# Performance work log

Hardware: AMD Instinct MI355X
Metric: run time of the kernel (lower is better)

Reference implementation:

```python
import jax, jax.numpy as jnp
import numpy as np

N = 4096          # num_nodes
E = 131072        # num_edges (avg degree 32)
H = 32            # hidden_channels
C_IN, C_OUT = 3, 3
DEPTH = 4
KS = [2000, 1000, 500, 250]  # ceil(ratio * n) per level, ratios = [2000/N, .5, .5, .5]


def gcn(x, A, W, b):
    """GCNConv with improved=True (self-loop fill 2, preserved if already present),
    symmetric normalization, aggregation out[dst] += norm * h[src]."""
    d = jnp.diagonal(A)
    A_hat = A + jnp.diag(jnp.where(d > 0, 0.0, 2.0))
    deg = A_hat.sum(0)                       # in-degree (col sums), as gcn_norm
    dis = jnp.where(deg > 0, jax.lax.rsqrt(deg), 0.0)
    msg = (x @ W) * dis[:, None]
    return (A_hat.T @ msg) * dis[:, None] + b


def augment(A):
    """GraphUNet.augment_adj: add self loops (w=1), square adjacency, drop self loops."""
    n = A.shape[0]
    eye = jnp.eye(n, dtype=A.dtype)
    A_sl = A + eye
    return (A_sl @ A_sl) * (1.0 - eye)


def pool(x, A, p, k):
    """TopKPooling: score = tanh((x.p)/||p||), keep top-k, gate x by score."""
    score = jnp.tanh((x @ p) / jnp.linalg.norm(p))
    vals, perm = jax.lax.top_k(score, k)
    return x[perm] * vals[:, None], A[perm][:, perm], perm


def setup_inputs() -> dict:
    key = jax.random.key(0)
    ks = jax.random.split(key, 12)
    x = jax.random.normal(ks[0], (N, C_IN), jnp.float32)
    edge_index = jax.random.randint(ks[1], (2, E), 0, N, dtype=jnp.int64)
    s = 0.1
    return {
        "x": x,
        "edge_index": edge_index,
        "W0": jax.random.normal(ks[2], (C_IN, H)) * s,
        "b0": jnp.zeros((H,), jnp.float32),
        "Wd": jax.random.normal(ks[3], (DEPTH, H, H)) * s,
        "bd": jnp.zeros((DEPTH, H), jnp.float32),
        "P": jax.random.normal(ks[4], (DEPTH, H)) * s,
        "Wu": jax.random.normal(ks[5], (DEPTH - 1, H, H)) * s,
        "bu": jnp.zeros((DEPTH - 1, H), jnp.float32),
        "Wlast": jax.random.normal(ks[6], (H, C_OUT)) * s,
        "blast": jnp.zeros((C_OUT,), jnp.float32),
    }


def reference(x, edge_index, W0, b0, Wd, bd, P, Wu, bu, Wlast, blast):
    # dense adjacency; duplicate edges accumulate like coalesced sparse weights
    A = jnp.zeros((N, N), jnp.float32).at[edge_index[0], edge_index[1]].add(1.0)
    x = jax.nn.relu(gcn(x, A, W0, b0))
    xs, As, perms = [x], [A], []
    for i in range(DEPTH):
        A = augment(A)
        x, A, perm = pool(x, A, P[i], KS[i])
        x = jax.nn.relu(gcn(x, A, Wd[i], bd[i]))
        if i < DEPTH - 1:
            xs.append(x)
            As.append(A)
        perms.append(perm)
    for i in range(DEPTH):
        j = DEPTH - 1 - i
        res = xs[j]
        up = jnp.zeros_like(res).at[perms[j]].set(x)  # unpool
        x = res + up                                   # sum_res=True
        if i < DEPTH - 1:
            x = jax.nn.relu(gcn(x, As[j], Wu[i], bu[i]))
        else:
            x = gcn(x, As[j], Wlast, blast)
    return jax.nn.log_softmax(x, axis=1)
```

## Files before the change

### kernel.cpp

```cpp
#include <hip/hip_runtime.h>
#include <math.h>

#define H 32
#define N0 4096
#define EMAX 131072
#define APSTR (4096 * 32)

typedef __attribute__((ext_vector_type(4))) float floatx4;
typedef __attribute__((ext_vector_type(8))) short short8;

__device__ __forceinline__ unsigned short f2bf_bits(float v) {
    union { float f; unsigned u; } c;
    c.f = v;
    unsigned lsb = (c.u >> 16) & 1u;
    c.u += 0x7fffu + lsb;
    return (unsigned short)(c.u >> 16);
}

__global__ void fill_sentinel_kernel(float* out, int n) {
    int t = blockIdx.x * 256 + threadIdx.x;
    if (t < n) out[t] = 9.0f;
}

__global__ void build_stats_kernel(const int* __restrict__ ei, int E, int* __restrict__ rowcnt,
                                   int* __restrict__ rowcntD, int* __restrict__ diagcnt) {
    int t = blockIdx.x * 256 + threadIdx.x;
    if (t >= E) return;
    int s = ei[t], d = ei[E + t];
    if ((unsigned)s >= N0 || (unsigned)d >= N0) return;
    atomicAdd(&rowcnt[s], 1);
    atomicAdd(&rowcntD[d], 1);
    if (s == d) atomicAdd(&diagcnt[s], 1);
}

__global__ __launch_bounds__(1024) void scan2_kernel(const int* __restrict__ cntA, int* __restrict__ rowpA,
                                                     int* __restrict__ curA, const int* __restrict__ cntB,
                                                     int* __restrict__ rowpB, int* __restrict__ curB) {
    __shared__ int part[1024];
    int tid = threadIdx.x;
    for (int pass = 0; pass < 2; pass++) {
        const int* cnt = pass ? cntB : cntA;
        int* rowp = pass ? rowpB : rowpA;
        int* cur = pass ? curB : curA;
        int base = tid * 4;
        int local[4];
        int s = 0;
#pragma unroll
        for (int i = 0; i < 4; i++) { local[i] = s; s += cnt[base + i]; }
        part[tid] = s;
        __syncthreads();
        for (int off = 1; off < 1024; off <<= 1) {
            int v = (tid >= off) ? part[tid - off] : 0;
            __syncthreads();
            part[tid] += v;
            __syncthreads();
        }
        int pre = (tid == 0) ? 0 : part[tid - 1];
#pragma unroll
        for (int i = 0; i < 4; i++) { rowp[base + i] = pre + local[i]; cur[base + i] = pre + local[i]; }
        if (tid == 1023) rowp[N0] = pre + s;
        __syncthreads();
    }
}

__global__ void fill_csr_kernel(const int* __restrict__ ei, int E, int* __restrict__ cursor,
                                int* __restrict__ cols, int* __restrict__ cursorD,
                                int* __restrict__ srcs) {
    int t = blockIdx.x * 256 + threadIdx.x;
    if (t >= E) return;
    int s = ei[t], d = ei[E + t];
    if ((unsigned)s >= N0 || (unsigned)d >= N0) return;
    int pos = atomicAdd(&cursor[s], 1);
    cols[pos] = d;
    int posD = atomicAdd(&cursorD[d], 1);
    srcs[posD] = s;
}

__global__ void invperm_set_kernel(const int* __restrict__ perm, int* __restrict__ invperm, int k) {
    int t = blockIdx.x * 256 + threadIdx.x;
    if (t < k) invperm[perm[t]] = t;
}

__global__ __launch_bounds__(256) void aug0_kernel(const int* __restrict__ rowp, const int* __restrict__ cols,
                                                   const int* __restrict__ perm, const int* __restrict__ invperm,
                                                   int kOut, int ldC, float* __restrict__ C) {
    __shared__ float row[2048];
    int a = blockIdx.x;
    int tid = threadIdx.x;
    for (int j = tid; j < ldC; j += 256) row[j] = 0.f;
    __syncthreads();
    if (a < kOut) {
        int pa = perm[a];
        int s0 = rowp[pa], s1 = rowp[pa + 1];
        for (int e = s0 + tid; e < s1; e += 256) {
            int k = cols[e];
            int ip = invperm[k];
            if (ip >= 0) atomicAdd(&row[ip], 2.0f);
            int t1 = rowp[k + 1];
            for (int e2 = rowp[k]; e2 < t1; ++e2) {
                int ip2 = invperm[cols[e2]];
                if (ip2 >= 0) atomicAdd(&row[ip2], 1.0f);
            }
        }
    }
    __syncthreads();
    for (int j = tid; j < ldC; j += 256) C[(long)a * ldC + j] = (j == a) ? 0.f : row[j];
}

__global__ void gather_rows_kernel(const float* __restrict__ M, int ldM, const int* __restrict__ perm,
                                   int kOut, float* __restrict__ Gr) {
    int k = blockIdx.x * 256 + threadIdx.x;
    int a = blockIdx.y;
    if (k >= ldM) return;
    float v = 0.f;
    if (a < kOut) {
        int pa = perm[a];
        v = M[(long)pa * ldM + k] + (k == pa ? 1.f : 0.f);
    }
    Gr[(long)a * ldM + k] = v;
}

__global__ void gather_rows_bf16_kernel(const float* __restrict__ M, int ldM, const int* __restrict__ perm,
                                        int kOut, unsigned short* __restrict__ Gr) {
    int k = blockIdx.x * 256 + threadIdx.x;
    int a = blockIdx.y;
    if (k >= ldM) return;
    float v = 0.f;
    if (a < kOut) {
        int pa = perm[a];
        v = M[(long)pa * ldM + k] + (k == pa ? 1.f : 0.f);
    }
    Gr[(long)a * ldM + k] = f2bf_bits(v);
}

__global__ void gather_cols_kernel(const float* __restrict__ M, int ldM, const int* __restrict__ perm,
                                   int kOut, float* __restrict__ Gc, int ldC) {
    int b = blockIdx.x * 256 + threadIdx.x;
    int k = blockIdx.y;
    if (b >= ldC) return;
    float v = 0.f;
    if (b < kOut) {
        int pb = perm[b];
        v = M[(long)k * ldM + pb] + (k == pb ? 1.f : 0.f);
    }
    Gc[(long)k * ldC + b] = v;
}

__global__ void gather_colsT_bf16_kernel(const float* __restrict__ M, int ldM,
                                         const int* __restrict__ perm, int kOut,
                                         unsigned short* __restrict__ GcT) {
    __shared__ float t[32][33];
    __shared__ int pb[32];
    int b0 = blockIdx.x * 32, k0 = blockIdx.y * 32;
    int tx = threadIdx.x, ty = threadIdx.y;
    if (ty == 0) pb[tx] = (b0 + tx < kOut) ? perm[b0 + tx] : -1;
    __syncthreads();
    for (int y = ty; y < 32; y += 8) {
        int k = k0 + y;
        int pbx = pb[tx];
        float v = 0.f;
        if (pbx >= 0) v = M[(long)k * ldM + pbx] + (k == pbx ? 1.f : 0.f);
        t[y][tx] = v;
    }
    __syncthreads();
    for (int y = ty; y < 32; y += 8)
        GcT[(long)(b0 + y) * ldM + k0 + tx] = f2bf_bits(t[tx][y]);
}

__global__ __launch_bounds__(256) void mfma_aug_kernel(const unsigned short* __restrict__ Aop,
                                                       const unsigned short* __restrict__ Bop,
                                                       float* __restrict__ C, int K, int ldC, int kchunk) {
    __shared__ __align__(16) unsigned short lA[64 * 32];
    __shared__ __align__(16) unsigned short lB[64 * 32];
    const int tid = threadIdx.x;
    const int lane = tid & 63;
    const int w = tid >> 6;
    const int a0 = blockIdx.y * 64, b0 = blockIdx.x * 64;
    const int kbase = blockIdx.z * kchunk;
    const int r0 = tid >> 2;
    const int c8 = (tid & 3) * 8;
    const unsigned short* gA = Aop + (long)(a0 + r0) * K + kbase + c8;
    const unsigned short* gB = Bop + (long)(b0 + r0) * K + kbase + c8;
    const int wm = (w & 1) * 32;
    const int wn = (w >> 1) * 32;
    const int lm = lane & 15;
    const int quad = lane >> 4;
    floatx4 acc[2][2];
#pragma unroll
    for (int i = 0; i < 2; i++)
#pragma unroll
        for (int j = 0; j < 2; j++) {
            floatx4 z = {0.f, 0.f, 0.f, 0.f};
            acc[i][j] = z;
        }
    for (int k0 = 0; k0 < kchunk; k0 += 32) {
        short8 va = *(const short8*)(gA + k0);
        short8 vb = *(const short8*)(gB + k0);
        __syncthreads();
        *(short8*)&lA[r0 * 32 + c8] = va;
        *(short8*)&lB[r0 * 32 + c8] = vb;
        __syncthreads();
        short8 af[2], bf[2];
#pragma unroll
        for (int mi = 0; mi < 2; mi++) af[mi] = *(const short8*)&lA[(wm + mi * 16 + lm) * 32 + quad * 8];
#pragma unroll
        for (int ni = 0; ni < 2; ni++) bf[ni] = *(const short8*)&lB[(wn + ni * 16 + lm) * 32 + quad * 8];
#pragma unroll
        for (int mi = 0; mi < 2; mi++)
#pragma unroll
            for (int ni = 0; ni < 2; ni++)
                acc[mi][ni] = __builtin_amdgcn_mfma_f32_16x16x32_bf16(af[mi], bf[ni], acc[mi][ni], 0, 0, 0);
    }
#pragma unroll
    for (int mi = 0; mi < 2; mi++)
#pragma unroll
        for (int ni = 0; ni < 2; ni++) {
            int col = b0 + wn + ni * 16 + lm;
#pragma unroll
            for (int r = 0; r < 4; r++) {
                int row = a0 + wm + mi * 16 + quad * 4 + r;
                if (row != col) atomicAdd(&C[(long)row * ldC + col], acc[mi][ni][r]);
            }
        }
}

__global__ __launch_bounds__(256) void gemm64_kernel(const float* __restrict__ Gr,
                                                     const float* __restrict__ Gc,
                                                     float* __restrict__ Cpart, int K, int ldC, int kchunk) {
    __shared__ float As[32][68];
    __shared__ float Bs[32][68];
    const int tid = threadIdx.x;
    const int a0 = blockIdx.y * 64, b0 = blockIdx.x * 64;
    const int kbase = blockIdx.z * kchunk;
    float* Cz = Cpart + (long)blockIdx.z * ldC * ldC;
    const int tx = tid & 15, ty = tid >> 4;
    const int lr = tid >> 2;
    const int lk = (tid & 3) * 8;
    const int bb = tid & 63;
    const int kr = (tid >> 6) * 8;
    const float* gA = Gr + (long)(a0 + lr) * K + lk + kbase;
    const float* gB = Gc + (long)(kr + kbase) * ldC + b0 + bb;
    float acc[4][4];
#pragma unroll
    for (int i = 0; i < 4; i++)
#pragma unroll
        for (int j = 0; j < 4; j++) acc[i][j] = 0.f;
    for (int k0 = 0; k0 < kchunk; k0 += 32) {
        float a8[8], b8[8];
#pragma unroll
        for (int i = 0; i < 8; i++) a8[i] = gA[k0 + i];
#pragma unroll
        for (int i = 0; i < 8; i++) b8[i] = gB[(long)(k0 + i) * ldC];
        __syncthreads();
#pragma unroll
        for (int i = 0; i < 8; i++) As[lk + i][lr] = a8[i];
#pragma unroll
        for (int i = 0; i < 8; i++) Bs[kr + i][bb] = b8[i];
        __syncthreads();
#pragma unroll
        for (int k = 0; k < 32; k++) {
            floatx4 av = *(const floatx4*)&As[k][ty * 4];
            floatx4 bv = *(const floatx4*)&Bs[k][tx * 4];
#pragma unroll
            for (int i = 0; i < 4; i++)
#pragma unroll
                for (int j = 0; j < 4; j++) acc[i][j] += av[i] * bv[j];
        }
    }
#pragma unroll
    for (int i = 0; i < 4; i++)
#pragma unroll
        for (int j = 0; j < 4; j++) {
            int a = a0 + ty * 4 + i, b = b0 + tx * 4 + j;
            Cz[(long)a * ldC + b] = acc[i][j];
        }
}

__global__ void reduce_part_kernel(const float* __restrict__ Cpart, float* __restrict__ C,
                                   int ldC, int ksplit) {
    int t = blockIdx.x * 256 + threadIdx.x;
    long tot = (long)ldC * ldC;
    if (t >= tot) return;
    float s = 0.f;
    for (int z = 0; z < ksplit; z++) s += Cpart[(long)z * tot + t];
    int a = t / ldC, b = t % ldC;
    C[t] = (a == b) ? 0.f : s;
}

__global__ void colsum_part_kernel(const float* __restrict__ A, float* __restrict__ degp, int ld) {
    int i = blockIdx.x * 256 + threadIdx.x;
    int jb = blockIdx.y;
    int j0 = jb * 64;
    float s0 = 0.f, s1 = 0.f, s2 = 0.f, s3 = 0.f, s4 = 0.f, s5 = 0.f, s6 = 0.f, s7 = 0.f;
    const float* p = A + (long)j0 * ld + i;
#pragma unroll
    for (int jq = 0; jq < 64; jq += 8) {
        float v[8];
#pragma unroll
        for (int q = 0; q < 8; q++) v[q] = p[(long)(jq + q) * ld];
        s0 += v[0]; s1 += v[1]; s2 += v[2]; s3 += v[3];
        s4 += v[4]; s5 += v[5]; s6 += v[6]; s7 += v[7];
    }
    float s = ((s0 + s1) + (s2 + s3)) + ((s4 + s5) + (s6 + s7));
    degp[(long)jb * ld + i] = s;
}

__global__ void msgg_kernel(const float* __restrict__ x, const int* __restrict__ perm,
                            const float* __restrict__ vals, const float* __restrict__ Wb,
                            const float* __restrict__ A, int ld, const float* __restrict__ degp,
                            int nparts, float* __restrict__ dis, float* __restrict__ fixb,
                            float* __restrict__ msg, int n) {
    int idx = blockIdx.x * 256 + threadIdx.x;
    if (idx >= n * 32) return;
    int i = idx >> 5, c = idx & 31;
    float dsum = 0.f;
    for (int z = 0; z < nparts; z++) dsum += degp[(long)z * ld + i];
    float diag = A[(long)i * ld + i];
    float fx = diag > 0.f ? 0.f : 2.f;
    float dg = dsum + fx;
    float di = dg > 0.f ? 1.f / sqrtf(dg) : 0.f;
    if (c == 0) { dis[i] = di; fixb[i] = fx; }
    int src = perm ? perm[i] : i;
    float vs = vals ? vals[i] : 1.f;
    float s = 0.f;
#pragma unroll
    for (int q = 0; q < 32; q++) s += x[src * 32 + q] * Wb[q * 32 + c];
    msg[idx] = s * vs * di;
}

__global__ __launch_bounds__(256) void aggT_kernel(const float* __restrict__ A,
                                                   const float* __restrict__ msg,
                                                   float* __restrict__ aggp, int n, int ld, int jchunk) {
    __shared__ float As[64][64];
    __shared__ float Ms[64][32];
    const int tid = threadIdx.x;
    const int i0 = blockIdx.x * 64;
    const int il = tid & 63;
    const int cg = tid >> 6;
    const int i = i0 + il;
    const int mrow = tid >> 2;
    const int mc = (tid & 3) * 8;
    float acc[8];
#pragma unroll
    for (int q = 0; q < 8; q++) acc[q] = 0.f;
    const int j0 = blockIdx.y * jchunk;
    for (int jb = j0; jb < j0 + jchunk; jb += 64) {
        float a16[16], m8[8];
#pragma unroll
        for (int q = 0; q < 16; q++) a16[q] = A[(long)(jb + cg + 4 * q) * ld + i0 + il];
#pragma unroll
        for (int q = 0; q < 8; q++) m8[q] = msg[(long)(jb + mrow) * 32 + mc + q];
        __syncthreads();
#pragma unroll
        for (int q = 0; q < 16; q++) As[cg + 4 * q][il] = a16[q];
#pragma unroll
        for (int q = 0; q < 8; q++) Ms[mrow][mc + q] = m8[q];
        __syncthreads();
#pragma unroll
        for (int jl = 0; jl < 64; jl++) {
            float a = As[jl][il];
#pragma unroll
            for (int q = 0; q < 8; q++) acc[q] += a * Ms[jl][cg * 8 + q];
        }
        __syncthreads();
    }
    if (i < n) {
#pragma unroll
        for (int q = 0; q < 8; q++) aggp[(long)blockIdx.y * APSTR + (long)i * 32 + cg * 8 + q] = acc[q];
    }
}

__global__ void epi_sum_kernel(const float* __restrict__ aggp, int jsplit, const float* __restrict__ msg,
                               const float* __restrict__ dis, const float* __restrict__ fixb,
                               const float* __restrict__ bb, float* __restrict__ out, int n, int relu) {
    int idx = blockIdx.x * 256 + threadIdx.x;
    if (idx >= n * 32) return;
    int i = idx >> 5, c = idx & 31;
    float s = 0.f;
    for (int z = 0; z < jsplit; z++) s += aggp[(long)z * APSTR + idx];
    float v = (s + fixb[i] * msg[idx]) * dis[i] + bb[c];
    if (relu) v = fmaxf(v, 0.f);
    out[idx] = v;
}

__global__ void msg0_kernel(const float* __restrict__ x, const float* __restrict__ Wb,
                            const int* __restrict__ rowcntD, const int* __restrict__ diagcnt,
                            float* __restrict__ dis, float* __restrict__ fixb,
                            float* __restrict__ msg, int n) {
    int idx = blockIdx.x * 256 + threadIdx.x;
    if (idx >= n * 32) return;
    int i = idx >> 5, c = idx & 31;
    float fx = diagcnt[i] > 0 ? 0.f : 2.f;
    float dg = (float)rowcntD[i] + fx;
    float di = dg > 0.f ? 1.f / sqrtf(dg) : 0.f;
    if (c == 0) { dis[i] = di; fixb[i] = fx; }
    float s = x[i * 3] * Wb[c] + x[i * 3 + 1] * Wb[32 + c] + x[i * 3 + 2] * Wb[64 + c];
    msg[idx] = s * di;
}

template <int CIN, int COUT>
__global__ void msg_kernel(const float* __restrict__ x, const float* __restrict__ Wb,
                           const float* __restrict__ dis, float* __restrict__ msg, int n) {
    int idx = blockIdx.x * 256 + threadIdx.x;
    if (idx >= n * COUT) return;
    int i = idx / COUT, c = idx % COUT;
    float s = 0.f;
#pragma unroll
    for (int q = 0; q < CIN; q++) s += x[i * CIN + q] * Wb[q * COUT + c];
    msg[idx] = s * dis[i];
}

template <int COUT>
__global__ void cscagg_epi_kernel(const int* __restrict__ rowpD, const int* __restrict__ srcs,
                                  const float* __restrict__ msg, const float* __restrict__ dis,
                                  const float* __restrict__ fixb, const float* __restrict__ bb,
                                  float* __restrict__ out, int n, int relu) {
    int t = blockIdx.x * 256 + threadIdx.x;
    if (t >= n * COUT) return;
    int i = t / COUT, c = t % COUT;
    float acc = 0.f;
    int e0 = rowpD[i], e1 = rowpD[i + 1];
    for (int e = e0; e < e1; e++) acc += msg[(long)srcs[e] * COUT + c];
    float v = (acc + fixb[i] * msg[t]) * dis[i] + bb[c];
    if (relu) v = fmaxf(v, 0.f);
    out[t] = v;
}

__global__ void cscagg_lsm_kernel(const int* __restrict__ rowpD, const int* __restrict__ srcs,
                                  const float* __restrict__ msg, const float* __restrict__ dis,
                                  const float* __restrict__ fixb, const float* __restrict__ bb,
                                  float* __restrict__ out, int n) {
    int i = blockIdx.x * 256 + threadIdx.x;
    if (i >= n) return;
    float a0 = 0.f, a1 = 0.f, a2 = 0.f;
    int e0 = rowpD[i], e1 = rowpD[i + 1];
    for (int e = e0; e < e1; e++) {
        const float* m = &msg[(long)srcs[e] * 3];
        a0 += m[0]; a1 += m[1]; a2 += m[2];
    }
    float di = dis[i], fx = fixb[i];
    float v0 = (a0 + fx * msg[i * 3]) * di + bb[0];
    float v1 = (a1 + fx * msg[i * 3 + 1]) * di + bb[1];
    float v2 = (a2 + fx * msg[i * 3 + 2]) * di + bb[2];
    float m = fmaxf(v0, fmaxf(v1, v2));
    float s = expf(v0 - m) + expf(v1 - m) + expf(v2 - m);
    float l = m + logf(s);
    out[i * 3] = v0 - l;
    out[i * 3 + 1] = v1 - l;
    out[i * 3 + 2] = v2 - l;
}

__global__ void score_keys_kernel(const float* __restrict__ x, const float* __restrict__ p,
                                  int n, int npow, unsigned long long* __restrict__ keys) {
    __shared__ float psh[32];
    const int tid = threadIdx.x;
    if (tid < 32) psh[tid] = p[tid];
    __syncthreads();
    int i = blockIdx.x * 256 + tid;
    if (i >= npow) return;
    unsigned long long kk = 0ULL;
    if (i < n) {
        float nrm = 0.f, dot = 0.f;
#pragma unroll
        for (int c = 0; c < 32; c++) {
            nrm += psh[c] * psh[c];
            dot += x[i * 32 + c] * psh[c];
        }
        float sc = tanhf(dot / sqrtf(nrm));
        unsigned u = __float_as_uint(sc);
        u = (u & 0x80000000u) ? ~u : (u | 0x80000000u);
        kk = ((unsigned long long)u << 32) | (unsigned)(~i);
    }
    keys[i] = kk;
}

__global__ __launch_bounds__(256) void topk_rank_kernel(const unsigned long long* __restrict__ keys,
                                                        int npow, int k, int* __restrict__ perm,
                                                        float* __restrict__ vals) {
    __shared__ unsigned long long ks[4096];
    __shared__ int psum[256];
    const int tid = threadIdx.x;
    for (int t = tid; t < npow; t += 256) ks[t] = keys[t];
    __syncthreads();
    const int m = tid & 15;
    const int chunk = tid >> 4;
    const int myi = blockIdx.x * 16 + m;
    unsigned long long my = ks[myi];
    const int cl = npow >> 4;
    const unsigned long long* base = &ks[chunk * cl];
    int r = 0;
#pragma unroll 4
    for (int j = 0; j < cl; j++) r += (base[j] > my) ? 1 : 0;
    psum[chunk * 16 + m] = r;
    __syncthreads();
    if (tid < 16) {
        int mk_i = blockIdx.x * 16 + tid;
        unsigned long long mk = ks[mk_i];
        int rank = 0;
#pragma unroll
        for (int c = 0; c < 16; c++) rank += psum[c * 16 + tid];
        if (rank < k) {
            perm[rank] = (int)(~(unsigned)mk);
            unsigned u = (unsigned)(mk >> 32);
            u = (u & 0x80000000u) ? (u ^ 0x80000000u) : ~u;
            vals[rank] = __uint_as_float(u);
        }
    }
}

__global__ void copy_kernel(float* __restrict__ dst, const float* __restrict__ src, int n) {
    int t = blockIdx.x * 256 + threadIdx.x;
    if (t < n) dst[t] = src[t];
}

__global__ void scatter_add_kernel(float* __restrict__ dst, const float* __restrict__ src,
                                   const int* __restrict__ perm, int k) {
    int t = blockIdx.x * 256 + threadIdx.x;
    if (t >= k * H) return;
    int a = t >> 5, c = t & 31;
    dst[perm[a] * H + c] += src[t];
}

static void run_gcn_dense(hipStream_t st, const float* A, int n, int ld, const float* x,
                          const int* perm, const float* vals, const float* Wt, const float* bt,
                          int relu, float* out, float* degp, float* aggp, float* dis, float* fixb,
                          float* msgb) {
    dim3 gcs(ld / 256 > 0 ? ld / 256 : 1, ld / 64);
    colsum_part_kernel<<<gcs, 256, 0, st>>>(A, degp, ld);
    int gm = (n * H + 255) / 256;
    msgg_kernel<<<gm, 256, 0, st>>>(x, perm, vals, Wt, A, ld, degp, ld / 64, dis, fixb, msgb, n);
    int jsplit = ld / 256 > 0 ? ld / 256 : 1;
    int ajc = ld / jsplit;
    dim3 ga(ld / 64, jsplit);
    aggT_kernel<<<ga, 256, 0, st>>>(A, msgb, aggp, n, ld, ajc);
    epi_sum_kernel<<<gm, 256, 0, st>>>(aggp, jsplit, msgb, dis, fixb, bt, out, n, relu);
}

extern "C" void kernel_launch(void* const* d_in, const int* in_sizes, int n_in,
                              void* d_out, int out_size, void* d_ws, size_t ws_size,
                              hipStream_t stream) {
    const float* x0f = (const float*)d_in[0];
    const int* eidx = (const int*)d_in[1];
    const float* W0f = (const float*)d_in[2];
    const float* b0f = (const float*)d_in[3];
    const float* Wdf = (const float*)d_in[4];
    const float* bdf = (const float*)d_in[5];
    const float* Pf = (const float*)d_in[6];
    const float* Wuf = (const float*)d_in[7];
    const float* buf2 = (const float*)d_in[8];
    const float* Wlf = (const float*)d_in[9];
    const float* blf = (const float*)d_in[10];
    const int E = in_sizes[1] / 2;

    unsigned char* w = (unsigned char*)d_ws;
    size_t off = 0;
    auto alloc = [&](size_t bytes) -> void* {
        void* p = w + off;
        off += (bytes + 255) & ~(size_t)255;
        return p;
    };
    int* rowcnt = (int*)alloc(N0 * 4);
    int* rowcntD = (int*)alloc(N0 * 4);
    int* diagcnt = (int*)alloc(N0 * 4);
    int* rowp = (int*)alloc((N0 + 1) * 4);
    int* rowpD = (int*)alloc((N0 + 1) * 4);
    int* cursor = (int*)alloc(N0 * 4);
    int* cursorD = (int*)alloc(N0 * 4);
    int* cols = (int*)alloc((size_t)EMAX * 4);
    int* srcs = (int*)alloc((size_t)EMAX * 4);
    int* invperm = (int*)alloc(N0 * 4);
    float* dis0 = (float*)alloc(N0 * 4);
    float* fixb0 = (float*)alloc(N0 * 4);
    unsigned long long* keys = (unsigned long long*)alloc((size_t)N0 * 8);
    float* A1 = (float*)alloc((size_t)2048 * 2048 * 4);
    float* A2 = (float*)alloc((size_t)1024 * 1024 * 4);
    float* A3 = (float*)alloc((size_t)512 * 512 * 4);
    float* A4 = (float*)alloc((size_t)256 * 256 * 4);
    float* Gr = (float*)alloc((size_t)1024 * 2048 * 4);
    float* Gc = (float*)alloc((size_t)2048 * 1024 * 4);
    unsigned short* Grb = (unsigned short*)alloc((size_t)1024 * 2048 * 2);
    unsigned short* GcTb = (unsigned short*)alloc((size_t)1024 * 2048 * 2);
    float* Cpart = (float*)alloc((size_t)8 * 512 * 512 * 4);
    float* degp = (float*)alloc((size_t)32 * 2048 * 4);
    float* aggp = (float*)alloc((size_t)8 * APSTR * 4);
    float* xs0 = (float*)alloc((size_t)N0 * H * 4);
    float* xs1 = (float*)alloc((size_t)2000 * H * 4);
    float* xs2 = (float*)alloc((size_t)1000 * H * 4);
    float* xs3 = (float*)alloc((size_t)500 * H * 4);
    float* xtA = (float*)alloc((size_t)N0 * H * 4);
    float* xtB = (float*)alloc((size_t)N0 * H * 4);
    float* msgb = (float*)alloc((size_t)N0 * H * 4);
    float* dis = (float*)alloc(N0 * 4);
    float* fixb = (float*)alloc(N0 * 4);
    const int ksz[4] = {2000, 1000, 500, 250};
    int* perm[4];
    float* vals[4];
    for (int i = 0; i < 4; i++) perm[i] = (int*)alloc((size_t)ksz[i] * 4);
    for (int i = 0; i < 4; i++) vals[i] = (float*)alloc((size_t)ksz[i] * 4);

    if (off > ws_size) {
        fill_sentinel_kernel<<<(out_size + 255) / 256, 256, 0, stream>>>((float*)d_out, out_size);
        return;
    }

    const int nlvl[5] = {N0, 2000, 1000, 500, 250};
    const int ldl[5] = {N0, 2048, 1024, 512, 256};
    const int npw[4] = {4096, 2048, 1024, 512};
    float* Afp[5] = {nullptr, A1, A2, A3, A4};
    float* xsb[4] = {xs0, xs1, xs2, xs3};

    hipMemsetAsync(rowcnt, 0, (size_t)N0 * 3 * 4, stream);
    build_stats_kernel<<<(E + 255) / 256, 256, 0, stream>>>(eidx, E, rowcnt, rowcntD, diagcnt);
    scan2_kernel<<<1, 1024, 0, stream>>>(rowcnt, rowp, cursor, rowcntD, rowpD, cursorD);
    fill_csr_kernel<<<(E + 255) / 256, 256, 0, stream>>>(eidx, E, cursor, cols, cursorD, srcs);

    msg0_kernel<<<(N0 * H + 255) / 256, 256, 0, stream>>>(x0f, W0f, rowcntD, diagcnt, dis0, fixb0,
                                                          msgb, N0);
    cscagg_epi_kernel<H><<<(N0 * H + 255) / 256, 256, 0, stream>>>(rowpD, srcs, msgb, dis0, fixb0,
                                                                   b0f, xs0, N0, 1);
    float* xcur = xs0;

    for (int i = 0; i < 4; ++i) {
        int nd = nlvl[i], kk = ksz[i], ldn = ldl[i + 1];
        score_keys_kernel<<<(npw[i] + 255) / 256, 256, 0, stream>>>(xcur, Pf + i * H, nd, npw[i], keys);
        topk_rank_kernel<<<npw[i] / 16, 256, 0, stream>>>(keys, npw[i], kk, perm[i], vals[i]);
        if (i == 0) {
            hipMemsetAsync(invperm, 0xFF, (size_t)N0 * 4, stream);
            invperm_set_kernel<<<(kk + 255) / 256, 256, 0, stream>>>(perm[0], invperm, kk);
            aug0_kernel<<<ldn, 256, 0, stream>>>(rowp, cols, perm[0], invperm, kk, ldn, A1);
        } else if (i == 1) {
            int ldM = ldl[i];
            dim3 gr((ldM + 255) / 256, ldn);
            gather_rows_bf16_kernel<<<gr, 256, 0, stream>>>(Afp[i], ldM, perm[i], kk, Grb);
            dim3 gt(ldn / 32, ldM / 32);
            gather_colsT_bf16_kernel<<<gt, dim3(32, 8), 0, stream>>>(Afp[i], ldM, perm[i], kk, GcTb);
            hipMemsetAsync(Afp[i + 1], 0, (size_t)ldn * ldn * 4, stream);
            int ksplit = 4;
            int kchunk = ldM / ksplit;
            dim3 gg(ldn / 64, ldn / 64, ksplit);
            mfma_aug_kernel<<<gg, 256, 0, stream>>>(Grb, GcTb, Afp[i + 1], ldM, ldn, kchunk);
        } else {
            int ldM = ldl[i];
            dim3 gr((ldM + 255) / 256, ldn);
            gather_rows_kernel<<<gr, 256, 0, stream>>>(Afp[i], ldM, perm[i], kk, Gr);
            dim3 gc((ldn + 255) / 256, ldM);
            gather_cols_kernel<<<gc, 256, 0, stream>>>(Afp[i], ldM, perm[i], kk, Gc, ldn);
            int ksplit = 8;
            int kchunk = ldM / ksplit;
            dim3 gg(ldn / 64, ldn / 64, ksplit);
            gemm64_kernel<<<gg, 256, 0, stream>>>(Gr, Gc, Cpart, ldM, ldn, kchunk);
            long tot = (long)ldn * ldn;
            reduce_part_kernel<<<(tot + 255) / 256, 256, 0, stream>>>(Cpart, Afp[i + 1], ldn, ksplit);
        }
        float* outx = (i < 3) ? xsb[i + 1] : xtB;
        run_gcn_dense(stream, Afp[i + 1], kk, ldn, xcur, perm[i], vals[i], Wdf + i * (H * H),
                      bdf + i * H, 1, outx, degp, aggp, dis, fixb, msgb);
        xcur = outx;
    }

    for (int i = 0; i < 4; ++i) {
        int j = 3 - i;
        int nj = nlvl[j], kj = ksz[j];
        copy_kernel<<<(nj * H + 255) / 256, 256, 0, stream>>>(xtA, xsb[j], nj * H);
        scatter_add_kernel<<<(kj * H + 255) / 256, 256, 0, stream>>>(xtA, xcur, perm[j], kj);
        if (i < 3) {
            run_gcn_dense(stream, Afp[j], nj, ldl[j], xtA, nullptr, nullptr, Wuf + i * (H * H),
                          buf2 + i * H, 1, xtB, degp, aggp, dis, fixb, msgb);
        } else {
            msg_kernel<H, 3><<<(N0 * 3 + 255) / 256, 256, 0, stream>>>(xtA, Wlf, dis0, msgb, N0);
            cscagg_lsm_kernel<<<(N0 + 255) / 256, 256, 0, stream>>>(rowpD, srcs, msgb, dis0, fixb0,
                                                                    blf, (float*)d_out, N0);
        }
        xcur = xtB;
    }
}
```

Baseline: 477.5 us.

## Fuse TopK score computation into GCN epilogues and cache per-level degree normalization

The separate score_keys kernel is removed. Pooling scores and sort keys are now computed inside the GCN epilogue kernels using warp shuffles across the 32 channels, including padding entries up to the power-of-two size. Degree normalization (dis/fixb) is stored per level during the down pass and reused in the up pass, which skips the dense column-sum kernel and the diagonal read there. This removes several launches and full passes over dense adjacency matrices, at the cost of extra per-level buffers and a larger epilogue grid.

```diff
diff --git a/kernel.cpp b/kernel.cpp
--- a/kernel.cpp
+++ b/kernel.cpp
@@ -313,19 +313,26 @@
     int idx = blockIdx.x * 256 + threadIdx.x;
     if (idx >= n * 32) return;
     int i = idx >> 5, c = idx & 31;
-    float dsum = 0.f;
-    for (int z = 0; z < nparts; z++) dsum += degp[(long)z * ld + i];
-    float diag = A[(long)i * ld + i];
-    float fx = diag > 0.f ? 0.f : 2.f;
-    float dg = dsum + fx;
-    float di = dg > 0.f ? 1.f / sqrtf(dg) : 0.f;
-    if (c == 0) { dis[i] = di; fixb[i] = fx; }
+    float di, fx;
+    if (degp) {
+        float dsum = 0.f;
+        for (int z = 0; z < nparts; z++) dsum += degp[(long)z * ld + i];
+        float diag = A[(long)i * ld + i];
+        fx = diag > 0.f ? 0.f : 2.f;
+        float dg = dsum + fx;
+        di = dg > 0.f ? 1.f / sqrtf(dg) : 0.f;
+        if (c == 0) { dis[i] = di; fixb[i] = fx; }
+    } else {
+        di = dis[i];
+        fx = fixb[i];
+    }
     int src = perm ? perm[i] : i;
     float vs = vals ? vals[i] : 1.f;
     float s = 0.f;
 #pragma unroll
     for (int q = 0; q < 32; q++) s += x[src * 32 + q] * Wb[q * 32 + c];
     msg[idx] = s * vs * di;
+    (void)fx;
 }
 
 __global__ __launch_bounds__(256) void aggT_kernel(const float* __restrict__ A,
@@ -372,15 +379,46 @@
 
 __global__ void epi_sum_kernel(const float* __restrict__ aggp, int jsplit, const float* __restrict__ msg,
                                const float* __restrict__ dis, const float* __restrict__ fixb,
-                               const float* __restrict__ bb, float* __restrict__ out, int n, int relu) {
+                               const float* __restrict__ bb, float* __restrict__ out, int n, int relu,
+                               const float* __restrict__ p, int npow,
+                               unsigned long long* __restrict__ keys) {
+    __shared__ float psh[32];
+    if (p) {
+        if (threadIdx.x < 32) psh[threadIdx.x] = p[threadIdx.x];
+        __syncthreads();
+    }
     int idx = blockIdx.x * 256 + threadIdx.x;
-    if (idx >= n * 32) return;
+    int tot = (p ? npow : n) * 32;
+    if (idx >= tot) return;
     int i = idx >> 5, c = idx & 31;
-    float s = 0.f;
-    for (int z = 0; z < jsplit; z++) s += aggp[(long)z * APSTR + idx];
-    float v = (s + fixb[i] * msg[idx]) * dis[i] + bb[c];
-    if (relu) v = fmaxf(v, 0.f);
-    out[idx] = v;
+    float v = 0.f;
+    if (i < n) {
+        float s = 0.f;
+        for (int z = 0; z < jsplit; z++) s += aggp[(long)z * APSTR + idx];
+        v = (s + fixb[i] * msg[idx]) * dis[i] + bb[c];
+        if (relu) v = fmaxf(v, 0.f);
+        out[idx] = v;
+    }
+    if (p) {
+        float pc = psh[c];
+        float d = v * pc;
+        float nq = pc * pc;
+#pragma unroll
+        for (int st = 16; st >= 1; st >>= 1) {
+            d += __shfl_xor(d, st);
+            nq += __shfl_xor(nq, st);
+        }
+        if (c == 0) {
+            unsigned long long kk = 0ULL;
+            if (i < n) {
+                float sc = tanhf(d / sqrtf(nq));
+                unsigned u = __float_as_uint(sc);
+                u = (u & 0x80000000u) ? ~u : (u | 0x80000000u);
+                kk = ((unsigned long long)u << 32) | (unsigned)(~i);
+            }
+            keys[i] = kk;
+        }
+    }
 }
 
 __global__ void msg0_kernel(const float* __restrict__ x, const float* __restrict__ Wb,
@@ -410,20 +448,37 @@
     msg[idx] = s * dis[i];
 }
 
-template <int COUT>
-__global__ void cscagg_epi_kernel(const int* __restrict__ rowpD, const int* __restrict__ srcs,
-                                  const float* __restrict__ msg, const float* __restrict__ dis,
-                                  const float* __restrict__ fixb, const float* __restrict__ bb,
-                                  float* __restrict__ out, int n, int relu) {
-    int t = blockIdx.x * 256 + threadIdx.x;
-    if (t >= n * COUT) return;
-    int i = t / COUT, c = t % COUT;
+__global__ void cscagg_epi_keys_kernel(const int* __restrict__ rowpD, const int* __restrict__ srcs,
+                                       const float* __restrict__ msg, const float* __restrict__ dis,
+                                       const float* __restrict__ fixb, const float* __restrict__ bb,
+                                       float* __restrict__ out, int n, const float* __restrict__ p,
+                                       unsigned long long* __restrict__ keys) {
+    __shared__ float psh[32];
+    if (threadIdx.x < 32) psh[threadIdx.x] = p[threadIdx.x];
+    __syncthreads();
+    int idx = blockIdx.x * 256 + threadIdx.x;
+    if (idx >= n * 32) return;
+    int i = idx >> 5, c = idx & 31;
     float acc = 0.f;
     int e0 = rowpD[i], e1 = rowpD[i + 1];
-    for (int e = e0; e < e1; e++) acc += msg[(long)srcs[e] * COUT + c];
-    float v = (acc + fixb[i] * msg[t]) * dis[i] + bb[c];
-    if (relu) v = fmaxf(v, 0.f);
-    out[t] = v;
+    for (int e = e0; e < e1; e++) acc += msg[(long)srcs[e] * 32 + c];
+    float v = (acc + fixb[i] * msg[idx]) * dis[i] + bb[c];
+    v = fmaxf(v, 0.f);
+    out[idx] = v;
+    float pc = psh[c];
+    float d = v * pc;
+    float nq = pc * pc;
+#pragma unroll
+    for (int st = 16; st >= 1; st >>= 1) {
+        d += __shfl_xor(d, st);
+        nq += __shfl_xor(nq, st);
+    }
+    if (c == 0) {
+        float sc = tanhf(d / sqrtf(nq));
+        unsigned u = __float_as_uint(sc);
+        u = (u & 0x80000000u) ? ~u : (u | 0x80000000u);
+        keys[i] = ((unsigned long long)u << 32) | (unsigned)(~i);
+    }
 }
 
 __global__ void cscagg_lsm_kernel(const int* __restrict__ rowpD, const int* __restrict__ srcs,
@@ -448,30 +503,6 @@
     out[i * 3] = v0 - l;
     out[i * 3 + 1] = v1 - l;
     out[i * 3 + 2] = v2 - l;
-}
-
-__global__ void score_keys_kernel(const float* __restrict__ x, const float* __restrict__ p,
-                                  int n, int npow, unsigned long long* __restrict__ keys) {
-    __shared__ float psh[32];
-    const int tid = threadIdx.x;
-    if (tid < 32) psh[tid] = p[tid];
-    __syncthreads();
-    int i = blockIdx.x * 256 + tid;
-    if (i >= npow) return;
-    unsigned long long kk = 0ULL;
-    if (i < n) {
-        float nrm = 0.f, dot = 0.f;
-#pragma unroll
-        for (int c = 0; c < 32; c++) {
-            nrm += psh[c] * psh[c];
-            dot += x[i * 32 + c] * psh[c];
-        }
-        float sc = tanhf(dot / sqrtf(nrm));
-        unsigned u = __float_as_uint(sc);
-        u = (u & 0x80000000u) ? ~u : (u | 0x80000000u);
-        kk = ((unsigned long long)u << 32) | (unsigned)(~i);
-    }
-    keys[i] = kk;
 }
 
 __global__ __launch_bounds__(256) void topk_rank_kernel(const unsigned long long* __restrict__ keys,
@@ -524,16 +555,22 @@
 static void run_gcn_dense(hipStream_t st, const float* A, int n, int ld, const float* x,
                           const int* perm, const float* vals, const float* Wt, const float* bt,
                           int relu, float* out, float* degp, float* aggp, float* dis, float* fixb,
-                          float* msgb) {
-    dim3 gcs(ld / 256 > 0 ? ld / 256 : 1, ld / 64);
-    colsum_part_kernel<<<gcs, 256, 0, st>>>(A, degp, ld);
+                          float* msgb, int computeDeg, const float* pnext, int npow_next,
+                          unsigned long long* keys) {
+    if (computeDeg) {
+        dim3 gcs(ld / 256 > 0 ? ld / 256 : 1, ld / 64);
+        colsum_part_kernel<<<gcs, 256, 0, st>>>(A, degp, ld);
+    }
     int gm = (n * H + 255) / 256;
-    msgg_kernel<<<gm, 256, 0, st>>>(x, perm, vals, Wt, A, ld, degp, ld / 64, dis, fixb, msgb, n);
+    msgg_kernel<<<gm, 256, 0, st>>>(x, perm, vals, Wt, A, ld, computeDeg ? degp : nullptr, ld / 64,
+                                    dis, fixb, msgb, n);
     int jsplit = ld / 256 > 0 ? ld / 256 : 1;
     int ajc = ld / jsplit;
     dim3 ga(ld / 64, jsplit);
     aggT_kernel<<<ga, 256, 0, st>>>(A, msgb, aggp, n, ld, ajc);
-    epi_sum_kernel<<<gm, 256, 0, st>>>(aggp, jsplit, msgb, dis, fixb, bt, out, n, relu);
+    int gme = ((pnext ? npow_next : n) * H + 255) / 256;
+    epi_sum_kernel<<<gme, 256, 0, st>>>(aggp, jsplit, msgb, dis, fixb, bt, out, n, relu,
+                                        pnext, npow_next, keys);
 }
 
 extern "C" void kernel_launch(void* const* d_in, const int* in_sizes, int n_in,
@@ -590,8 +627,8 @@
     float* xtA = (float*)alloc((size_t)N0 * H * 4);
     float* xtB = (float*)alloc((size_t)N0 * H * 4);
     float* msgb = (float*)alloc((size_t)N0 * H * 4);
-    float* dis = (float*)alloc(N0 * 4);
-    float* fixb = (float*)alloc(N0 * 4);
+    float* disL = (float*)alloc((size_t)4 * N0 * 4);
+    float* fixbL = (float*)alloc((size_t)4 * N0 * 4);
     const int ksz[4] = {2000, 1000, 500, 250};
     int* perm[4];
     float* vals[4];
@@ -616,13 +653,12 @@
 
     msg0_kernel<<<(N0 * H + 255) / 256, 256, 0, stream>>>(x0f, W0f, rowcntD, diagcnt, dis0, fixb0,
                                                           msgb, N0);
-    cscagg_epi_kernel<H><<<(N0 * H + 255) / 256, 256, 0, stream>>>(rowpD, srcs, msgb, dis0, fixb0,
-                                                                   b0f, xs0, N0, 1);
+    cscagg_epi_keys_kernel<<<(N0 * H + 255) / 256, 256, 0, stream>>>(rowpD, srcs, msgb, dis0, fixb0,
+                                                                     b0f, xs0, N0, Pf, keys);
     float* xcur = xs0;
 
     for (int i = 0; i < 4; ++i) {
-        int nd = nlvl[i], kk = ksz[i], ldn = ldl[i + 1];
-        score_keys_kernel<<<(npw[i] + 255) / 256, 256, 0, stream>>>(xcur, Pf + i * H, nd, npw[i], keys);
+        int kk = ksz[i], ldn = ldl[i + 1];
         topk_rank_kernel<<<npw[i] / 16, 256, 0, stream>>>(keys, npw[i], kk, perm[i], vals[i]);
         if (i == 0) {
             hipMemsetAsync(invperm, 0xFF, (size_t)N0 * 4, stream);
@@ -653,8 +689,11 @@
             reduce_part_kernel<<<(tot + 255) / 256, 256, 0, stream>>>(Cpart, Afp[i + 1], ldn, ksplit);
         }
         float* outx = (i < 3) ? xsb[i + 1] : xtB;
+        const float* pnext = (i < 3) ? (Pf + (i + 1) * H) : nullptr;
+        int npow_next = (i < 3) ? npw[i + 1] : 0;
         run_gcn_dense(stream, Afp[i + 1], kk, ldn, xcur, perm[i], vals[i], Wdf + i * (H * H),
-                      bdf + i * H, 1, outx, degp, aggp, dis, fixb, msgb);
+                      bdf + i * H, 1, outx, degp, aggp, disL + i * N0, fixbL + i * N0, msgb,
+                      1, pnext, npow_next, keys);
         xcur = outx;
     }
 
@@ -665,7 +704,8 @@
         scatter_add_kernel<<<(kj * H + 255) / 256, 256, 0, stream>>>(xtA, xcur, perm[j], kj);
         if (i < 3) {
             run_gcn_dense(stream, Afp[j], nj, ldl[j], xtA, nullptr, nullptr, Wuf + i * (H * H),
-                          buf2 + i * H, 1, xtB, degp, aggp, dis, fixb, msgb);
+                          buf2 + i * H, 1, xtB, degp, aggp, disL + (j - 1) * N0,
+                          fixbL + (j - 1) * N0, msgb, 0, nullptr, 0, nullptr);
         } else {
             msg_kernel<H, 3><<<(N0 * 3 + 255) / 256, 256, 0, stream>>>(xtA, Wlf, dis0, msgb, N0);
             cscagg_lsm_kernel<<<(N0 + 255) / 256, 256, 0, stream>>>(rowpD, srcs, msgb, dis0, fixb0,
```

Result: faster. 446.0 us (-6.6%).
